# Performance work log

Measured on AMD Instinct MI355X. Metric: run time of the kernel, lower is better.

The kernel has to match this reference:

```python
import jax, jax.numpy as jnp
import numpy as np

N_PER, B, D, CIN, COUT = 500000, 2, 192, 64, 64
EPS = 1e-5


def _build_coords_and_nbrs():
    rng = np.random.default_rng(0)
    cells, xs, ys, zs = [], [], [], []
    for b in range(B):
        cell = rng.choice(D ** 3, size=N_PER, replace=False).astype(np.int64)
        cells.append(cell + b * D ** 3)
        xs.append(cell // (D * D))
        ys.append((cell // D) % D)
        zs.append(cell % D)
    lin = np.concatenate(cells)
    x = np.concatenate(xs); y = np.concatenate(ys); z = np.concatenate(zs)
    N = lin.shape[0]
    order = np.argsort(lin)
    slin = lin[order]

    def nbrs(axis_stride, cvals):
        cols = []
        for d in (-1, 0, 1):
            tgt = lin + d * axis_stride
            valid = (cvals + d >= 0) & (cvals + d < D)
            pos = np.searchsorted(slin, tgt)
            pc = np.clip(pos, 0, N - 1)
            found = valid & (slin[pc] == tgt)
            cols.append(np.where(found, order[pc], -1))
        return np.stack(cols, axis=1).astype(np.int32)  # [N,3]

    return nbrs(1, z), nbrs(D, y), nbrs(D * D, x)


def setup_inputs() -> dict:
    key = jax.random.key(0)
    k1, k2, k3, k4 = jax.random.split(key, 4)
    nbr_z, nbr_y, nbr_x = _build_coords_and_nbrs()
    N = B * N_PER
    s = 1.0 / np.sqrt(3.0 * CIN)
    return {
        "feats": jax.random.normal(k1, (N, CIN), jnp.float32),
        "W1": jax.random.normal(k2, (3, CIN, CIN), jnp.float32) * s,
        "W2": jax.random.normal(k3, (3, CIN, CIN), jnp.float32) * s,
        "W3": jax.random.normal(k4, (3, CIN, COUT), jnp.float32) * s,
        "gamma": jnp.ones((COUT,), jnp.float32),
        "beta": jnp.zeros((COUT,), jnp.float32),
        "nbr_z": jnp.asarray(nbr_z),
        "nbr_y": jnp.asarray(nbr_y),
        "nbr_x": jnp.asarray(nbr_x),
    }


def _sparse_conv1d(feats, W, nbr):
    # feats [N,Cin], W [3,Cin,Cout], nbr [N,3] (-1 = missing neighbor)
    mask = (nbr >= 0)
    g = feats[jnp.where(mask, nbr, 0)]              # [N,3,Cin] gather
    g = g * mask[..., None].astype(feats.dtype)     # zero missing taps
    return jnp.einsum('nkc,kcd->nd', g, W)          # GEMM over taps


def reference(feats, W1, W2, W3, gamma, beta, nbr_z, nbr_y, nbr_x):
    h = _sparse_conv1d(feats, W1, nbr_z)   # conv (1,1,3)
    h = _sparse_conv1d(h, W2, nbr_y)       # conv (1,3,1)
    h = _sparse_conv1d(h, W3, nbr_x)       # conv (3,1,1)
    # BatchNorm over the N active points (training-mode batch stats)
    mean = jnp.mean(h, axis=0)
    var = jnp.var(h, axis=0)
    h = (h - mean) * (gamma / jnp.sqrt(var + EPS)) + beta
    return jax.nn.relu(h)
```

## Files before the change

### kernel.cpp

```cpp
#include <hip/hip_runtime.h>
#include <cstdint>
#include <cstddef>


typedef __attribute__((ext_vector_type(4))) float float4v;
typedef __attribute__((ext_vector_type(4))) unsigned int uint4v;
typedef __attribute__((ext_vector_type(8))) __bf16 bf16x8;
typedef __attribute__((ext_vector_type(8))) unsigned short ushort8;

__device__ __forceinline__ unsigned short f2bf_bits(float f) {
    unsigned int u = __builtin_bit_cast(unsigned int, f);
    u += 0x7fffu + ((u >> 16) & 1u);
    return (unsigned short)(u >> 16);
}
__device__ __forceinline__ float bf2f(unsigned short b) {
    unsigned int u = ((unsigned int)b) << 16;
    return __builtin_bit_cast(float, u);
}

__device__ __forceinline__ void stage_W(const float* __restrict__ Wg,
                                        unsigned short* __restrict__ Bld, int tid)
{
    for (int i = tid; i < 192 * 64; i += 256) {
        int kc = i >> 6, d = i & 63;
        int tap = kc >> 6, c = kc & 63;
        int s  = tap * 2 + (c >> 5);
        int qd = (c >> 3) & 3, j = c & 7;
        int ln = qd * 16 + (d & 15);
        Bld[(((s * 4 + (d >> 4)) * 64 + ln) << 3) + j] = f2bf_bits(Wg[i]);
    }
}

__device__ __forceinline__ void mfma_tap(const unsigned short* __restrict__ Bld,
                                         int lane, bf16x8 a0, bf16x8 a1, int s0,
                                         float4v (&acc)[4])
{
#pragma unroll
    for (int nt = 0; nt < 4; ++nt) {
        uint4v ub = *reinterpret_cast<const uint4v*>(
            Bld + (((s0 * 4 + nt) * 64 + lane) << 3));
        acc[nt] = __builtin_amdgcn_mfma_f32_16x16x32_bf16(
            a0, __builtin_bit_cast(bf16x8, ub), acc[nt], 0, 0, 0);
    }
#pragma unroll
    for (int nt = 0; nt < 4; ++nt) {
        uint4v ub = *reinterpret_cast<const uint4v*>(
            Bld + ((((s0 + 1) * 4 + nt) * 64 + lane) << 3));
        acc[nt] = __builtin_amdgcn_mfma_f32_16x16x32_bf16(
            a1, __builtin_bit_cast(bf16x8, ub), acc[nt], 0, 0, 0);
    }
}

template<bool DO_STATS>
__device__ __forceinline__ void tile_epilogue(const float4v (&acc)[4],
    unsigned short* __restrict__ tl, unsigned short* __restrict__ Hout,
    int t, int lane, int l15, int quad, float (&lsum)[4], float (&lsq)[4])
{
    if (DO_STATS) {
#pragma unroll
        for (int nt = 0; nt < 4; ++nt) {
            lsum[nt] += acc[nt][0] + acc[nt][1] + acc[nt][2] + acc[nt][3];
            lsq[nt]  += acc[nt][0] * acc[nt][0] + acc[nt][1] * acc[nt][1]
                      + acc[nt][2] * acc[nt][2] + acc[nt][3] * acc[nt][3];
        }
    }
#pragma unroll
    for (int nt = 0; nt < 4; ++nt)
#pragma unroll
        for (int r = 0; r < 4; ++r)
            tl[(quad * 4 + r) * 72 + nt * 16 + l15] = f2bf_bits(acc[nt][r]);
    __asm__ volatile("s_waitcnt lgkmcnt(0)" ::: "memory");
    unsigned short* op = Hout + ((size_t)t << 10);
#pragma unroll
    for (int c = 0; c < 2; ++c) {
        int chunk = c * 64 + lane;
        int r = chunk >> 3;
        int off = (chunk & 7) * 8;
        uint4v v = *reinterpret_cast<const uint4v*>(&tl[r * 72 + off]);
        *reinterpret_cast<uint4v*>(op + (r << 6) + off) = v;
    }
    __asm__ volatile("s_waitcnt lgkmcnt(0)" ::: "memory");
}


__device__ __forceinline__ void issue_bf16(
    uint4v (&A)[6], const char* __restrict__ abase,
    const char* __restrict__ zaddr, int i0, int i2, int t, int l15, int quad)
{
    const int qo = quad * 16;
    const char* g0 = (i0 >= 0) ? abase + (((size_t)(unsigned)i0) << 7) : zaddr;
    const char* gs = abase + (((size_t)(unsigned)(t * 16 + l15)) << 7);
    const char* g2 = (i2 >= 0) ? abase + (((size_t)(unsigned)i2) << 7) : zaddr;
    A[0] = *reinterpret_cast<const uint4v*>(g0 + qo);
    A[1] = *reinterpret_cast<const uint4v*>(g0 + qo + 64);
    A[2] = *reinterpret_cast<const uint4v*>(gs + qo);
    A[3] = *reinterpret_cast<const uint4v*>(gs + qo + 64);
    A[4] = *reinterpret_cast<const uint4v*>(g2 + qo);
    A[5] = *reinterpret_cast<const uint4v*>(g2 + qo + 64);
}

template<bool DO_STATS>
__device__ __forceinline__ void consume_bf16(
    const uint4v (&A)[6], int fl, const unsigned short* __restrict__ Bld,
    unsigned short* __restrict__ tl, unsigned short* __restrict__ Hout,
    int t, int lane, int l15, int quad, float (&lsum)[4], float (&lsq)[4])
{
    float4v acc[4] = {};
    if (fl & 1)
        mfma_tap(Bld, lane, __builtin_bit_cast(bf16x8, A[0]),
                 __builtin_bit_cast(bf16x8, A[1]), 0, acc);
    mfma_tap(Bld, lane, __builtin_bit_cast(bf16x8, A[2]),
             __builtin_bit_cast(bf16x8, A[3]), 2, acc);
    if (fl & 2)
        mfma_tap(Bld, lane, __builtin_bit_cast(bf16x8, A[4]),
                 __builtin_bit_cast(bf16x8, A[5]), 4, acc);
    tile_epilogue<DO_STATS>(acc, tl, Hout, t, lane, l15, quad, lsum, lsq);
}

template<bool DO_STATS>
__global__ __launch_bounds__(256, 4)
void conv_kernel(const unsigned short* __restrict__ Ain,
                 const float* __restrict__ Wg,
                 const int* __restrict__ nbr,
                 unsigned short* __restrict__ Hout,
                 const unsigned short* __restrict__ Zrow,
                 float* __restrict__ stats, int ntiles)
{
    __shared__ unsigned short Bld[24 * 64 * 8];
    __shared__ unsigned short Tld[4][16 * 72];
    __shared__ float ssum[64], ssq[64];

    const int tid = threadIdx.x;
    stage_W(Wg, Bld, tid);
    if (DO_STATS && tid < 64) { ssum[tid] = 0.f; ssq[tid] = 0.f; }
    __syncthreads();

    const int lane = tid & 63;
    const int wid  = tid >> 6;
    const int l15  = lane & 15;
    const int quad = lane >> 4;
    const char* abase = (const char*)Ain;
    const char* zaddr = (const char*)Zrow;
    unsigned short* tl = Tld[wid];

    float lsum[4] = {0.f, 0.f, 0.f, 0.f};
    float lsq[4]  = {0.f, 0.f, 0.f, 0.f};

    const int S = gridDim.x * 4;
    int t = blockIdx.x * 4 + wid;
    if (t < ntiles) {
        uint4v Aa[6], Ab[6];
        int flA = 0, flB = 0;
        int iN0 = 0, iN2 = 0;
        {
            size_t nb = (size_t)(t * 16 + l15) * 3;
            int i0 = nbr[nb], i2 = nbr[nb + 2];
            flA = (__any(i0 >= 0) ? 1 : 0) | (__any(i2 >= 0) ? 2 : 0);
            issue_bf16(Aa, abase, zaddr, i0, i2, t, l15, quad);
        }
        int tn = t + S;
        if (tn < ntiles) {
            size_t nb = (size_t)(tn * 16 + l15) * 3;
            iN0 = nbr[nb]; iN2 = nbr[nb + 2];
        }
        while (true) {
            int t2 = tn + S;
            if (tn < ntiles) {
                flB = (__any(iN0 >= 0) ? 1 : 0) | (__any(iN2 >= 0) ? 2 : 0);
                issue_bf16(Ab, abase, zaddr, iN0, iN2, tn, l15, quad);
            }
            if (t2 < ntiles) {
                size_t nb = (size_t)(t2 * 16 + l15) * 3;
                iN0 = nbr[nb]; iN2 = nbr[nb + 2];
            }
            consume_bf16<DO_STATS>(Aa, flA, Bld, tl, Hout, t, lane, l15, quad, lsum, lsq);
            t = tn; tn = t2;
            if (t >= ntiles) break;

            t2 = tn + S;
            if (tn < ntiles) {
                flA = (__any(iN0 >= 0) ? 1 : 0) | (__any(iN2 >= 0) ? 2 : 0);
                issue_bf16(Aa, abase, zaddr, iN0, iN2, tn, l15, quad);
            }
            if (t2 < ntiles) {
                size_t nb = (size_t)(t2 * 16 + l15) * 3;
                iN0 = nbr[nb]; iN2 = nbr[nb + 2];
            }
            consume_bf16<DO_STATS>(Ab, flB, Bld, tl, Hout, t, lane, l15, quad, lsum, lsq);
            t = tn; tn = t2;
            if (t >= ntiles) break;
        }
    }

    if (DO_STATS) {
#pragma unroll
        for (int nt = 0; nt < 4; ++nt) {
            atomicAdd(&ssum[nt * 16 + l15], lsum[nt]);
            atomicAdd(&ssq[nt * 16 + l15], lsq[nt]);
        }
        __syncthreads();
        if (tid < 64)               atomicAdd(&stats[tid], ssum[tid]);
        else if (tid < 128)         atomicAdd(&stats[tid], ssq[tid - 64]);
    }
}


__device__ __forceinline__ void issue_f32(
    uint4v (&R)[12], const char* __restrict__ fbase,
    const char* __restrict__ zaddr, int i0, int i2, int t, int l15, int quad)
{
    const int qo = quad * 32;
    const char* g0 = (i0 >= 0) ? fbase + ((size_t)(unsigned)i0) * 256 : zaddr;
    const char* gs = fbase + ((size_t)(unsigned)(t * 16 + l15)) * 256;
    const char* g2 = (i2 >= 0) ? fbase + ((size_t)(unsigned)i2) * 256 : zaddr;
    R[0]  = *reinterpret_cast<const uint4v*>(g0 + qo);
    R[1]  = *reinterpret_cast<const uint4v*>(g0 + qo + 16);
    R[2]  = *reinterpret_cast<const uint4v*>(g0 + qo + 128);
    R[3]  = *reinterpret_cast<const uint4v*>(g0 + qo + 144);
    R[4]  = *reinterpret_cast<const uint4v*>(gs + qo);
    R[5]  = *reinterpret_cast<const uint4v*>(gs + qo + 16);
    R[6]  = *reinterpret_cast<const uint4v*>(gs + qo + 128);
    R[7]  = *reinterpret_cast<const uint4v*>(gs + qo + 144);
    R[8]  = *reinterpret_cast<const uint4v*>(g2 + qo);
    R[9]  = *reinterpret_cast<const uint4v*>(g2 + qo + 16);
    R[10] = *reinterpret_cast<const uint4v*>(g2 + qo + 128);
    R[11] = *reinterpret_cast<const uint4v*>(g2 + qo + 144);
}

__device__ __forceinline__ bf16x8 pack_frag(uint4v lo, uint4v hi)
{
    float4v f0 = __builtin_bit_cast(float4v, lo);
    float4v f1 = __builtin_bit_cast(float4v, hi);
    ushort8 u;
#pragma unroll
    for (int j = 0; j < 4; ++j) {
        u[j]     = f2bf_bits(f0[j]);
        u[j + 4] = f2bf_bits(f1[j]);
    }
    return __builtin_bit_cast(bf16x8, u);
}

__device__ __forceinline__ void consume_f32(
    const uint4v (&R)[12], int fl, const unsigned short* __restrict__ Bld,
    unsigned short* __restrict__ tl, unsigned short* __restrict__ Hout,
    int t, int lane, int l15, int quad, float (&lsum)[4], float (&lsq)[4])
{
    float4v acc[4] = {};
    if (fl & 1)
        mfma_tap(Bld, lane, pack_frag(R[0], R[1]), pack_frag(R[2], R[3]), 0, acc);
    mfma_tap(Bld, lane, pack_frag(R[4], R[5]), pack_frag(R[6], R[7]), 2, acc);
    if (fl & 2)
        mfma_tap(Bld, lane, pack_frag(R[8], R[9]), pack_frag(R[10], R[11]), 4, acc);
    tile_epilogue<false>(acc, tl, Hout, t, lane, l15, quad, lsum, lsq);
}

__global__ __launch_bounds__(256, 3)
void conv1_kernel(const float* __restrict__ Fin,
                  const float* __restrict__ Wg,
                  const int* __restrict__ nbr,
                  unsigned short* __restrict__ Hout,
                  const float* __restrict__ Zrowf, int ntiles)
{
    __shared__ unsigned short Bld[24 * 64 * 8];
    __shared__ unsigned short Tld[4][16 * 72];

    const int tid = threadIdx.x;
    stage_W(Wg, Bld, tid);
    __syncthreads();

    const int lane = tid & 63;
    const int wid  = tid >> 6;
    const int l15  = lane & 15;
    const int quad = lane >> 4;
    const char* fbase = (const char*)Fin;
    const char* zaddr = (const char*)Zrowf;
    unsigned short* tl = Tld[wid];

    float lsum[4] = {0.f, 0.f, 0.f, 0.f};
    float lsq[4]  = {0.f, 0.f, 0.f, 0.f};

    const int S = gridDim.x * 4;
    int t = blockIdx.x * 4 + wid;
    if (t < ntiles) {
        uint4v Ra[12], Rb[12];
        int flA = 0, flB = 0;
        int iN0 = 0, iN2 = 0;
        {
            size_t nb = (size_t)(t * 16 + l15) * 3;
            int i0 = nbr[nb], i2 = nbr[nb + 2];
            flA = (__any(i0 >= 0) ? 1 : 0) | (__any(i2 >= 0) ? 2 : 0);
            issue_f32(Ra, fbase, zaddr, i0, i2, t, l15, quad);
        }
        int tn = t + S;
        if (tn < ntiles) {
            size_t nb = (size_t)(tn * 16 + l15) * 3;
            iN0 = nbr[nb]; iN2 = nbr[nb + 2];
        }
        while (true) {
            int t2 = tn + S;
            if (tn < ntiles) {
                flB = (__any(iN0 >= 0) ? 1 : 0) | (__any(iN2 >= 0) ? 2 : 0);
                issue_f32(Rb, fbase, zaddr, iN0, iN2, tn, l15, quad);
            }
            if (t2 < ntiles) {
                size_t nb = (size_t)(t2 * 16 + l15) * 3;
                iN0 = nbr[nb]; iN2 = nbr[nb + 2];
            }
            consume_f32(Ra, flA, Bld, tl, Hout, t, lane, l15, quad, lsum, lsq);
            t = tn; tn = t2;
            if (t >= ntiles) break;

            t2 = tn + S;
            if (tn < ntiles) {
                flA = (__any(iN0 >= 0) ? 1 : 0) | (__any(iN2 >= 0) ? 2 : 0);
                issue_f32(Ra, fbase, zaddr, iN0, iN2, tn, l15, quad);
            }
            if (t2 < ntiles) {
                size_t nb = (size_t)(t2 * 16 + l15) * 3;
                iN0 = nbr[nb]; iN2 = nbr[nb + 2];
            }
            consume_f32(Rb, flB, Bld, tl, Hout, t, lane, l15, quad, lsum, lsq);
            t = tn; tn = t2;
            if (t >= ntiles) break;
        }
    }
}


__global__ __launch_bounds__(256)
void bn_relu_kernel(const unsigned short* __restrict__ H,
                    const float* __restrict__ stats,
                    const float* __restrict__ gamma,
                    const float* __restrict__ beta,
                    float* __restrict__ out, size_t ntot, float invN)
{
    __shared__ float sscale[64], sbias[64];
    const int tid = threadIdx.x;
    if (tid < 64) {
        float mean = stats[tid] * invN;
        float var  = stats[tid + 64] * invN - mean * mean;
        float sc   = gamma[tid] * rsqrtf(var + 1e-5f);
        sscale[tid] = sc;
        sbias[tid]  = beta[tid] - mean * sc;
    }
    __syncthreads();
    size_t i0 = ((size_t)blockIdx.x * 256 + tid) * 8;
    const size_t stride = (size_t)gridDim.x * 2048;
    const int cb = (int)(i0 & 63);
    float sc[8], bs[8];
#pragma unroll
    for (int j = 0; j < 8; ++j) { sc[j] = sscale[cb + j]; bs[j] = sbias[cb + j]; }
    for (size_t i = i0; i < ntot; i += stride) {
        uint4v v = *reinterpret_cast<const uint4v*>(H + i);
        float4v o0, o1;
#pragma unroll
        for (int j = 0; j < 4; ++j) {
            float lo = bf2f((unsigned short)(v[j] & 0xffffu));
            float hi = bf2f((unsigned short)(v[j] >> 16));
            float r0 = fmaxf(lo * sc[2 * j]     + bs[2 * j],     0.f);
            float r1 = fmaxf(hi * sc[2 * j + 1] + bs[2 * j + 1], 0.f);
            if (j < 2) { o0[2 * j] = r0; o0[2 * j + 1] = r1; }
            else       { o1[2 * (j - 2)] = r0; o1[2 * (j - 2) + 1] = r1; }
        }
        *reinterpret_cast<float4v*>(out + i)     = o0;
        *reinterpret_cast<float4v*>(out + i + 4) = o1;
    }
}

extern "C" void kernel_launch(void* const* d_in, const int* in_sizes, int n_in,
                              void* d_out, int out_size, void* d_ws, size_t ws_size,
                              hipStream_t stream)
{
    const float* feats = (const float*)d_in[0];
    const float* W1    = (const float*)d_in[1];
    const float* W2    = (const float*)d_in[2];
    const float* W3    = (const float*)d_in[3];
    const float* gamma = (const float*)d_in[4];
    const float* beta  = (const float*)d_in[5];
    const int* nbr_z   = (const int*)d_in[6];
    const int* nbr_y   = (const int*)d_in[7];
    const int* nbr_x   = (const int*)d_in[8];

    const int N = in_sizes[0] / 64;
    const int ntiles = N / 16;

    char* ws = (char*)d_ws;
    float* stats = (float*)ws;
    float* zrowf = (float*)(ws + 512);
    unsigned short* zrow = (unsigned short*)(ws + 512);
    unsigned short* h1 = (unsigned short*)(ws + 1024);
    unsigned short* h2 = h1 + (size_t)N * 64;
    unsigned short* h3 = h2 + (size_t)N * 64;

    hipMemsetAsync(ws, 0, 1024, stream);

    dim3 blk(256);
    conv1_kernel<<<dim3(1024), blk, 0, stream>>>(feats, W1, nbr_z, h1, zrowf, ntiles);
    conv_kernel<false><<<dim3(1024), blk, 0, stream>>>(h1, W2, nbr_y, h2, zrow, nullptr, ntiles);
    conv_kernel<true ><<<dim3(1024), blk, 0, stream>>>(h2, W3, nbr_x, h3, zrow, stats, ntiles);
    bn_relu_kernel<<<dim3(8192), blk, 0, stream>>>(h3, stats, gamma, beta,
                                                   (float*)d_out, (size_t)N * 64,
                                                   1.0f / (float)N);
}
```

Baseline: 677.3 us.

## Deepen bf16 gather pipeline to three stages and drop epilogue LDS waits

The bf16 conv kernel's tile loop moves from double-buffered to triple-buffered register prefetch. Gathers for two tiles ahead are in flight while the current tile is consumed, and neighbor indices are loaded three tiles ahead. This is meant to hide more global gather latency, at the cost of higher VGPR pressure and possibly lower occupancy. It also removes the explicit s_waitcnt lgkmcnt(0) fences in the tile epilogue and relies on the compiler to order the per-wave LDS transpose writes and reads.

```diff
diff --git a/kernel.cpp b/kernel.cpp
--- a/kernel.cpp
+++ b/kernel.cpp
@@ -69,7 +69,6 @@
 #pragma unroll
         for (int r = 0; r < 4; ++r)
             tl[(quad * 4 + r) * 72 + nt * 16 + l15] = f2bf_bits(acc[nt][r]);
-    __asm__ volatile("s_waitcnt lgkmcnt(0)" ::: "memory");
     unsigned short* op = Hout + ((size_t)t << 10);
 #pragma unroll
     for (int c = 0; c < 2; ++c) {
@@ -79,7 +78,6 @@
         uint4v v = *reinterpret_cast<const uint4v*>(&tl[r * 72 + off]);
         *reinterpret_cast<uint4v*>(op + (r << 6) + off) = v;
     }
-    __asm__ volatile("s_waitcnt lgkmcnt(0)" ::: "memory");
 }
 
 
@@ -149,46 +147,70 @@
     const int S = gridDim.x * 4;
     int t = blockIdx.x * 4 + wid;
     if (t < ntiles) {
-        uint4v Aa[6], Ab[6];
-        int flA = 0, flB = 0;
-        int iN0 = 0, iN2 = 0;
+        uint4v A0[6], A1[6], A2[6];
+        int f0 = 0, f1 = 0, f2 = 0;
+        int ia = 0, ib = 0;
         {
             size_t nb = (size_t)(t * 16 + l15) * 3;
-            int i0 = nbr[nb], i2 = nbr[nb + 2];
-            flA = (__any(i0 >= 0) ? 1 : 0) | (__any(i2 >= 0) ? 2 : 0);
-            issue_bf16(Aa, abase, zaddr, i0, i2, t, l15, quad);
-        }
-        int tn = t + S;
-        if (tn < ntiles) {
-            size_t nb = (size_t)(tn * 16 + l15) * 3;
-            iN0 = nbr[nb]; iN2 = nbr[nb + 2];
+            int x = nbr[nb], y = nbr[nb + 2];
+            f0 = (__any(x >= 0) ? 1 : 0) | (__any(y >= 0) ? 2 : 0);
+            issue_bf16(A0, abase, zaddr, x, y, t, l15, quad);
+        }
+        int t1 = t + S;
+        if (t1 < ntiles) {
+            size_t nb = (size_t)(t1 * 16 + l15) * 3;
+            int x = nbr[nb], y = nbr[nb + 2];
+            f1 = (__any(x >= 0) ? 1 : 0) | (__any(y >= 0) ? 2 : 0);
+            issue_bf16(A1, abase, zaddr, x, y, t1, l15, quad);
+        }
+        int t2 = t1 + S;
+        if (t2 < ntiles) {
+            size_t nb = (size_t)(t2 * 16 + l15) * 3;
+            ia = nbr[nb]; ib = nbr[nb + 2];
         }
         while (true) {
-            int t2 = tn + S;
-            if (tn < ntiles) {
-                flB = (__any(iN0 >= 0) ? 1 : 0) | (__any(iN2 >= 0) ? 2 : 0);
-                issue_bf16(Ab, abase, zaddr, iN0, iN2, tn, l15, quad);
-            }
-            if (t2 < ntiles) {
-                size_t nb = (size_t)(t2 * 16 + l15) * 3;
-                iN0 = nbr[nb]; iN2 = nbr[nb + 2];
-            }
-            consume_bf16<DO_STATS>(Aa, flA, Bld, tl, Hout, t, lane, l15, quad, lsum, lsq);
-            t = tn; tn = t2;
-            if (t >= ntiles) break;
-
-            t2 = tn + S;
-            if (tn < ntiles) {
-                flA = (__any(iN0 >= 0) ? 1 : 0) | (__any(iN2 >= 0) ? 2 : 0);
-                issue_bf16(Aa, abase, zaddr, iN0, iN2, tn, l15, quad);
-            }
-            if (t2 < ntiles) {
-                size_t nb = (size_t)(t2 * 16 + l15) * 3;
-                iN0 = nbr[nb]; iN2 = nbr[nb + 2];
-            }
-            consume_bf16<DO_STATS>(Ab, flB, Bld, tl, Hout, t, lane, l15, quad, lsum, lsq);
-            t = tn; tn = t2;
-            if (t >= ntiles) break;
+            {
+                int t3 = t2 + S;
+                if (t2 < ntiles) {
+                    f2 = (__any(ia >= 0) ? 1 : 0) | (__any(ib >= 0) ? 2 : 0);
+                    issue_bf16(A2, abase, zaddr, ia, ib, t2, l15, quad);
+                }
+                if (t3 < ntiles) {
+                    size_t nb = (size_t)(t3 * 16 + l15) * 3;
+                    ia = nbr[nb]; ib = nbr[nb + 2];
+                }
+                consume_bf16<DO_STATS>(A0, f0, Bld, tl, Hout, t, lane, l15, quad, lsum, lsq);
+                t = t1; t1 = t2; t2 = t3;
+                if (t >= ntiles) break;
+            }
+            {
+                int t3 = t2 + S;
+                if (t2 < ntiles) {
+                    f0 = (__any(ia >= 0) ? 1 : 0) | (__any(ib >= 0) ? 2 : 0);
+                    issue_bf16(A0, abase, zaddr, ia, ib, t2, l15, quad);
+                }
+                if (t3 < ntiles) {
+                    size_t nb = (size_t)(t3 * 16 + l15) * 3;
+                    ia = nbr[nb]; ib = nbr[nb + 2];
+                }
+                consume_bf16<DO_STATS>(A1, f1, Bld, tl, Hout, t, lane, l15, quad, lsum, lsq);
+                t = t1; t1 = t2; t2 = t3;
+                if (t >= ntiles) break;
+            }
+            {
+                int t3 = t2 + S;
+                if (t2 < ntiles) {
+                    f1 = (__any(ia >= 0) ? 1 : 0) | (__any(ib >= 0) ? 2 : 0);
+                    issue_bf16(A1, abase, zaddr, ia, ib, t2, l15, quad);
+                }
+                if (t3 < ntiles) {
+                    size_t nb = (size_t)(t3 * 16 + l15) * 3;
+                    ia = nbr[nb]; ib = nbr[nb + 2];
+                }
+                consume_bf16<DO_STATS>(A2, f2, Bld, tl, Hout, t, lane, l15, quad, lsum, lsq);
+                t = t1; t1 = t2; t2 = t3;
+                if (t >= ntiles) break;
+            }
         }
     }
 
```

Result: slower. 835.7 us (+23.4%).
